# Optimization experiments

Measured on AMD Instinct MI355X. Metric: run time of the kernel, lower is better.

## Reference

```python
import jax, jax.numpy as jnp
import numpy as np

LATENT = 2048
PROJ = 128
N = 4096
TEMP = 0.5
BN_EPS = 1e-5
COS_EPS = 1e-8


def _batchnorm(x, gamma=None, beta=None):
    # training-mode BatchNorm1d: biased batch stats
    mean = jnp.mean(x, axis=0)
    var = jnp.mean((x - mean) ** 2, axis=0)
    xn = (x - mean) * jax.lax.rsqrt(var + BN_EPS)
    if gamma is not None:
        xn = xn * gamma + beta
    return xn


def _project(h, W1, gamma1, beta1, W2):
    x = h @ W1.T                      # [N, latent]
    x = jax.nn.relu(_batchnorm(x, gamma1, beta1))
    x = x @ W2.T                      # [N, proj]
    return _batchnorm(x)              # bn2 affine=False


def _normalize(z):
    n = jnp.linalg.norm(z, axis=-1, keepdims=True)
    return z / jnp.maximum(n, COS_EPS)


def setup_inputs() -> dict:
    key = jax.random.key(0)
    ks = jax.random.split(key, 4)
    scale_w1 = 1.0 / np.sqrt(LATENT)
    return {
        "h1": jax.random.normal(ks[0], (N, LATENT), jnp.float32),
        "h2": jax.random.normal(ks[1], (N, LATENT), jnp.float32),
        "W1": jax.random.normal(ks[2], (LATENT, LATENT), jnp.float32) * scale_w1,
        "gamma1": jnp.ones((LATENT,), jnp.float32),
        "beta1": jnp.zeros((LATENT,), jnp.float32),
        "W2": jax.random.normal(ks[3], (PROJ, LATENT), jnp.float32) * scale_w1,
    }


def reference(h1, h2, W1, gamma1, beta1, W2):
    z1 = _project(h1, W1, gamma1, beta1, W2)
    z2 = _project(h2, W1, gamma1, beta1, W2)
    zn1 = _normalize(z1)
    zn2 = _normalize(z2)
    inv_t = 1.0 / TEMP
    # cosine similarity as normalized GEMMs (same math as broadcast cossim)
    sim11 = (zn1 @ zn1.T) * inv_t      # [N, N]
    sim22 = (zn2 @ zn2.T) * inv_t
    sim12 = (zn1 @ zn2.T) * inv_t
    d = sim12.shape[-1]
    eye = jnp.eye(d, dtype=bool)
    neg_inf = jnp.float32(-jnp.inf)
    sim11 = jnp.where(eye, neg_inf, sim11)
    sim22 = jnp.where(eye, neg_inf, sim22)
    raw_scores1 = jnp.concatenate([sim12, sim11], axis=-1)       # [N, 2N]
    raw_scores2 = jnp.concatenate([sim22, sim12.T], axis=-1)     # [N, 2N]
    raw_scores = jnp.concatenate([raw_scores1, raw_scores2], axis=-2)  # [2N, 2N]
    targets = jnp.arange(2 * d, dtype=jnp.int64 if jax.config.jax_enable_x64 else jnp.int32)
    return raw_scores, targets
```

## Files before the change

kernel.cpp:

```cpp
#include <hip/hip_runtime.h>
#include <hip/hip_bf16.h>
#include <math.h>

#define NROWS 4096
#define MTOT  8192
#define LATENT 2048
#define PROJ 128
#define OUTN 8192
#define SPLITK 4
#define KWIN (LATENT / SPLITK)
#define CH2 256

using bf16 = __hip_bfloat16;
using bf16x8 = __attribute__((ext_vector_type(8))) short;
using bf16x4 = __attribute__((ext_vector_type(4))) short;
using f32x4  = __attribute__((ext_vector_type(4))) float;

#define LDS_AS(p) ((__attribute__((address_space(3))) void*)(p))
#define GLB_AS(p) ((const __attribute__((address_space(1))) void*)(p))

__device__ __forceinline__ float bf2f(short s) {
    return __uint_as_float(((unsigned)(unsigned short)s) << 16);
}
__device__ __forceinline__ short f2bf(float f) {
    bf16 h = __float2bfloat16(f);
    return __builtin_bit_cast(short, h);
}

__global__ void conv_all(const float* __restrict__ W1, const float* __restrict__ W2,
                         const float* __restrict__ h1, const float* __restrict__ h2,
                         bf16* __restrict__ W1b, bf16* __restrict__ W2b,
                         bf16* __restrict__ hb)
{
    const size_t g = ((size_t)blockIdx.x * 256 + threadIdx.x) * 8;
    const size_t N_W1 = (size_t)LATENT * LATENT;
    const size_t N_W2 = (size_t)PROJ * LATENT;
    const size_t N_H  = (size_t)NROWS * LATENT;
    const float* src; bf16* dst; size_t off;
    if (g < N_W1)                  { src = W1; dst = W1b;       off = g; }
    else if (g < N_W1 + N_W2)      { src = W2; dst = W2b;       off = g - N_W1; }
    else if (g < N_W1 + N_W2 + N_H){ src = h1; dst = hb;        off = g - N_W1 - N_W2; }
    else                           { src = h2; dst = hb + N_H;  off = g - N_W1 - N_W2 - N_H; }
    const float4 v0 = *reinterpret_cast<const float4*>(src + off);
    const float4 v1 = *reinterpret_cast<const float4*>(src + off + 4);
    bf16x8 o;
    o[0] = f2bf(v0.x); o[1] = f2bf(v0.y); o[2] = f2bf(v0.z); o[3] = f2bf(v0.w);
    o[4] = f2bf(v1.x); o[5] = f2bf(v1.y); o[6] = f2bf(v1.z); o[7] = f2bf(v1.w);
    *reinterpret_cast<bf16x8*>(dst + off) = o;
}

#define AREG(buf,kh) (sm + ((buf)*2 + (kh)) * 16384)
#define BREG(buf,kh) (sm + 65536 + ((buf)*2 + (kh)) * 16384)

#define LDA_(buf,kh,m) (*reinterpret_cast<const bf16x8*>(AREG(buf,kh) + (wr*128 + (m)*16 + fr)*64 + rslot))
#define LDB_(buf,kh,n) (*reinterpret_cast<const bf16x8*>(BREG(buf,kh) + (wc*64  + (n)*16 + fr)*64 + rslot))

#define STAGE_A(buf,kh,kt) do { \
    const bf16* g_ = Ag + (size_t)(bm + w*16 + srow) * 2048 + (kt)*64 + (kh)*32 + selem; \
    __builtin_amdgcn_global_load_lds(GLB_AS(g_),                  LDS_AS(AREG(buf,kh) + w*1024),        16, 0, 0); \
    __builtin_amdgcn_global_load_lds(GLB_AS(g_ + (size_t)128*2048), LDS_AS(AREG(buf,kh) + 8192 + w*1024), 16, 0, 0); \
} while(0)

#define STAGE_B(buf,kh,kt) do { \
    const bf16* g_ = Bg + (size_t)(bn + w*16 + srow) * 2048 + (kt)*64 + (kh)*32 + selem; \
    __builtin_amdgcn_global_load_lds(GLB_AS(g_),                  LDS_AS(BREG(buf,kh) + w*1024),        16, 0, 0); \
    __builtin_amdgcn_global_load_lds(GLB_AS(g_ + (size_t)128*2048), LDS_AS(BREG(buf,kh) + 8192 + w*1024), 16, 0, 0); \
} while(0)

#define PH(bufi, khi, mb, READB, STAGE_STMT, DO_VMCNT) do { \
    if (READB) { b0 = LDB_(bufi,khi,0); b1 = LDB_(bufi,khi,1); b2 = LDB_(bufi,khi,2); b3 = LDB_(bufi,khi,3); } \
    bf16x8 a0 = LDA_(bufi,khi,(mb)+0), a1 = LDA_(bufi,khi,(mb)+1), a2 = LDA_(bufi,khi,(mb)+2), a3 = LDA_(bufi,khi,(mb)+3); \
    STAGE_STMT; \
    __builtin_amdgcn_s_barrier(); \
    asm volatile("s_waitcnt lgkmcnt(0)" ::: "memory"); \
    __builtin_amdgcn_sched_barrier(0); \
    __builtin_amdgcn_s_setprio(1); \
    acc[(mb)+0][0] = __builtin_amdgcn_mfma_f32_16x16x32_bf16(b0, a0, acc[(mb)+0][0], 0,0,0); \
    acc[(mb)+0][1] = __builtin_amdgcn_mfma_f32_16x16x32_bf16(b1, a0, acc[(mb)+0][1], 0,0,0); \
    acc[(mb)+0][2] = __builtin_amdgcn_mfma_f32_16x16x32_bf16(b2, a0, acc[(mb)+0][2], 0,0,0); \
    acc[(mb)+0][3] = __builtin_amdgcn_mfma_f32_16x16x32_bf16(b3, a0, acc[(mb)+0][3], 0,0,0); \
    acc[(mb)+1][0] = __builtin_amdgcn_mfma_f32_16x16x32_bf16(b0, a1, acc[(mb)+1][0], 0,0,0); \
    acc[(mb)+1][1] = __builtin_amdgcn_mfma_f32_16x16x32_bf16(b1, a1, acc[(mb)+1][1], 0,0,0); \
    acc[(mb)+1][2] = __builtin_amdgcn_mfma_f32_16x16x32_bf16(b2, a1, acc[(mb)+1][2], 0,0,0); \
    acc[(mb)+1][3] = __builtin_amdgcn_mfma_f32_16x16x32_bf16(b3, a1, acc[(mb)+1][3], 0,0,0); \
    acc[(mb)+2][0] = __builtin_amdgcn_mfma_f32_16x16x32_bf16(b0, a2, acc[(mb)+2][0], 0,0,0); \
    acc[(mb)+2][1] = __builtin_amdgcn_mfma_f32_16x16x32_bf16(b1, a2, acc[(mb)+2][1], 0,0,0); \
    acc[(mb)+2][2] = __builtin_amdgcn_mfma_f32_16x16x32_bf16(b2, a2, acc[(mb)+2][2], 0,0,0); \
    acc[(mb)+2][3] = __builtin_amdgcn_mfma_f32_16x16x32_bf16(b3, a2, acc[(mb)+2][3], 0,0,0); \
    acc[(mb)+3][0] = __builtin_amdgcn_mfma_f32_16x16x32_bf16(b0, a3, acc[(mb)+3][0], 0,0,0); \
    acc[(mb)+3][1] = __builtin_amdgcn_mfma_f32_16x16x32_bf16(b1, a3, acc[(mb)+3][1], 0,0,0); \
    acc[(mb)+3][2] = __builtin_amdgcn_mfma_f32_16x16x32_bf16(b2, a3, acc[(mb)+3][2], 0,0,0); \
    acc[(mb)+3][3] = __builtin_amdgcn_mfma_f32_16x16x32_bf16(b3, a3, acc[(mb)+3][3], 0,0,0); \
    __builtin_amdgcn_s_setprio(0); \
    if (DO_VMCNT) { asm volatile("s_waitcnt vmcnt(6)" ::: "memory"); } \
    __builtin_amdgcn_s_barrier(); \
    __builtin_amdgcn_sched_barrier(0); \
} while (0)

__global__ __launch_bounds__(512, 2)
void gemm1_256(const bf16* __restrict__ Ag, const bf16* __restrict__ Bg,
               bf16* __restrict__ C, float* __restrict__ pS1, float* __restrict__ pSS1)
{
    extern __shared__ __align__(16) char sm[];

    const int t    = threadIdx.x;
    const int lane = t & 63;
    const int w    = t >> 6;
    const int wr   = w >> 2;
    const int wc   = w & 3;

    const int bid = blockIdx.x;
    const int lin = (bid & 7) * 32 + (bid >> 3);
    const int bm  = (lin & 31) * 256;
    const int bn  = (lin >> 5) * 256;

    const int srow  = lane >> 2;
    const int selem = 8 * ((lane & 3) ^ ((lane >> 2) & 3));
    const int fr    = lane & 15;
    const int rslot = 16 * ((lane >> 4) ^ (lane & 3));

    f32x4 acc[8][4];
#pragma unroll
    for (int m = 0; m < 8; ++m)
#pragma unroll
        for (int n = 0; n < 4; ++n)
#pragma unroll
            for (int r = 0; r < 4; ++r) acc[m][n][r] = 0.f;

    bf16x8 b0, b1, b2, b3;

    STAGE_B(0,0,0); STAGE_A(0,0,0); STAGE_B(0,1,0); STAGE_A(0,1,0);
    STAGE_B(1,0,1); STAGE_A(1,0,1); STAGE_B(1,1,1);
    asm volatile("s_waitcnt vmcnt(6)" ::: "memory");
    __builtin_amdgcn_s_barrier();
    __builtin_amdgcn_sched_barrier(0);

    for (int i = 0; i < 15; ++i) {
        const int kt1 = 2*i + 1, kt2 = 2*i + 2, kt3 = 2*i + 3;
        PH(0,0, 0, true,  STAGE_A(1,1,kt1), false);
        PH(0,0, 4, false, STAGE_B(0,0,kt2), false);
        PH(0,1, 0, true,  STAGE_A(0,0,kt2), false);
        PH(0,1, 4, false, STAGE_B(0,1,kt2), true);
        PH(1,0, 0, true,  STAGE_A(0,1,kt2), false);
        PH(1,0, 4, false, STAGE_B(1,0,kt3), false);
        PH(1,1, 0, true,  STAGE_A(1,0,kt3), false);
        PH(1,1, 4, false, STAGE_B(1,1,kt3), true);
    }

    STAGE_A(1,1,31);
    asm volatile("s_waitcnt vmcnt(0)" ::: "memory");
    __builtin_amdgcn_s_barrier();
    __builtin_amdgcn_sched_barrier(0);
    PH(0,0, 0, true,  ((void)0), false);
    PH(0,0, 4, false, ((void)0), false);
    PH(0,1, 0, true,  ((void)0), false);
    PH(0,1, 4, false, ((void)0), false);
    PH(1,0, 0, true,  ((void)0), false);
    PH(1,0, 4, false, ((void)0), false);
    PH(1,1, 0, true,  ((void)0), false);
    PH(1,1, 4, false, ((void)0), false);

    const int j_l = (lane >> 4) * 4;
#pragma unroll
    for (int m = 0; m < 8; ++m)
#pragma unroll
        for (int n = 0; n < 4; ++n) {
            const int crow = bm + wr * 128 + m * 16 + fr;
            const int ccol = bn + wc * 64 + n * 16 + j_l;
            bf16x4 o;
#pragma unroll
            for (int r = 0; r < 4; ++r) o[r] = f2bf(acc[m][n][r]);
            *reinterpret_cast<bf16x4*>(&C[(size_t)crow * LATENT + ccol]) = o;
        }

#pragma unroll
    for (int n = 0; n < 4; ++n)
#pragma unroll
        for (int r = 0; r < 4; ++r) {
            float sv = 0.f, qv = 0.f;
#pragma unroll
            for (int m = 0; m < 8; ++m) {
                const float v = acc[m][n][r];
                sv += v;
                qv = fmaf(v, v, qv);
            }
#pragma unroll
            for (int o = 1; o < 16; o <<= 1) {
                sv += __shfl_xor(sv, o);
                qv += __shfl_xor(qv, o);
            }
            if (fr == 0) {
                const int slot = ((bm >> 8) << 1) + wr;
                const int col  = bn + wc * 64 + n * 16 + j_l + r;
                pS1 [(size_t)slot * LATENT + col] = sv;
                pSS1[(size_t)slot * LATENT + col] = qv;
            }
        }
}

__global__ __launch_bounds__(512)
void gemm2_fused(const bf16* __restrict__ A, const bf16* __restrict__ B,
                 const float* __restrict__ pS1, const float* __restrict__ pSS1,
                 const float* __restrict__ gamma, const float* __restrict__ beta,
                 float* __restrict__ Part)
{
    __shared__ __align__(16) bf16 As[128 * 32];
    __shared__ __align__(16) bf16 Bs[128 * 32];
    __shared__ __align__(16) float sm_scale[KWIN];
    __shared__ __align__(16) float sm_shift[KWIN];

    const int kc = blockIdx.x;
    const int bm = blockIdx.y * 128;
    const int half = bm >> 12;
    const int kbeg = kc * KWIN;

    const int t    = threadIdx.x;
    const int lane = t & 63;
    const int w    = t >> 6;
    const int wrr  = w >> 2;
    const int wcc  = w & 3;

    {
        const int col = kbeg + t;
        float s = 0.f, ss = 0.f;
        for (int i = 0; i < 32; ++i) {
            s  += pS1 [((size_t)(half * 32 + i)) * LATENT + col];
            ss += pSS1[((size_t)(half * 32 + i)) * LATENT + col];
        }
        const float m    = s / NROWS;
        const float var  = ss / NROWS - m * m;
        const float rstd = 1.0f / sqrtf(var + 1e-5f);
        const float sc   = rstd * gamma[col];
        sm_scale[t] = sc;
        sm_shift[t] = beta[col] - m * sc;
    }
    __syncthreads();

    f32x4 acc[4][2];
#pragma unroll
    for (int m = 0; m < 4; ++m)
#pragma unroll
        for (int n = 0; n < 2; ++n)
#pragma unroll
            for (int r = 0; r < 4; ++r) acc[m][n][r] = 0.f;

    const int fr   = lane & 15;
    const int fk   = (lane >> 4) * 8;
    const int srow = t >> 2;
    const int scol = (t & 3) * 8;
    const int kend = kbeg + KWIN;

    for (int k0 = kbeg; k0 < kend; k0 += 32) {
        __builtin_amdgcn_global_load_lds(
            GLB_AS(&B[(size_t)(w * 16 + (lane >> 2)) * LATENT + k0 + (lane & 3) * 8]),
            LDS_AS(&Bs[w * 512]), 16, 0, 0);

        const int koff = k0 - kbeg;
        const float4 sc0 = *reinterpret_cast<const float4*>(&sm_scale[koff + scol]);
        const float4 sc1 = *reinterpret_cast<const float4*>(&sm_scale[koff + scol + 4]);
        const float4 sh0 = *reinterpret_cast<const float4*>(&sm_shift[koff + scol]);
        const float4 sh1 = *reinterpret_cast<const float4*>(&sm_shift[koff + scol + 4]);
        const float scv[8] = {sc0.x, sc0.y, sc0.z, sc0.w, sc1.x, sc1.y, sc1.z, sc1.w};
        const float shv[8] = {sh0.x, sh0.y, sh0.z, sh0.w, sh1.x, sh1.y, sh1.z, sh1.w};
        const bf16x8 av = *reinterpret_cast<const bf16x8*>(
            &A[(size_t)(bm + srow) * LATENT + k0 + scol]);
        bf16x8 o;
#pragma unroll
        for (int j = 0; j < 8; ++j)
            o[j] = f2bf(fmaxf(fmaf(bf2f(av[j]), scv[j], shv[j]), 0.f));
        *reinterpret_cast<bf16x8*>(&As[srow * 32 + scol]) = o;
        __syncthreads();

        bf16x8 a[4], b[2];
#pragma unroll
        for (int m = 0; m < 4; ++m)
            a[m] = *reinterpret_cast<const bf16x8*>(&As[(wrr * 64 + m * 16 + fr) * 32 + fk]);
#pragma unroll
        for (int n = 0; n < 2; ++n)
            b[n] = *reinterpret_cast<const bf16x8*>(&Bs[(wcc * 32 + n * 16 + fr) * 32 + fk]);

#pragma unroll
        for (int m = 0; m < 4; ++m)
#pragma unroll
            for (int n = 0; n < 2; ++n)
                acc[m][n] = __builtin_amdgcn_mfma_f32_16x16x32_bf16(b[n], a[m], acc[m][n], 0, 0, 0);
        __syncthreads();
    }

    const int i_l = lane & 15;
    const int j_l = (lane >> 4) * 4;
#pragma unroll
    for (int m = 0; m < 4; ++m)
#pragma unroll
        for (int n = 0; n < 2; ++n) {
            const int crow = bm + wrr * 64 + m * 16 + i_l;
            const int ccol = wcc * 32 + n * 16 + j_l;
            *reinterpret_cast<float4*>(&Part[((size_t)kc * MTOT + crow) * PROJ + ccol]) =
                make_float4(acc[m][n][0], acc[m][n][1], acc[m][n][2], acc[m][n][3]);
        }
}

__global__ __launch_bounds__(128)
void reduce2_kern(const float* __restrict__ Part, float* __restrict__ Z,
                  float* __restrict__ pS2, float* __restrict__ pSS2)
{
    const int c     = threadIdx.x;
    const int chunk = blockIdx.x;
    const int r0    = chunk * (MTOT / CH2);
    float s = 0.f, ss = 0.f;
    for (int r = r0; r < r0 + MTOT / CH2; ++r) {
        float z = 0.f;
#pragma unroll
        for (int kc = 0; kc < SPLITK; ++kc)
            z += Part[((size_t)kc * MTOT + r) * PROJ + c];
        Z[(size_t)r * PROJ + c] = z;
        s += z;
        ss = fmaf(z, z, ss);
    }
    pS2 [(size_t)chunk * PROJ + c] = s;
    pSS2[(size_t)chunk * PROJ + c] = ss;
}

__global__ __launch_bounds__(256)
void bn2_norm(const float* __restrict__ Z,
              const float* __restrict__ pS2, const float* __restrict__ pSS2,
              bf16* __restrict__ Zn, int* __restrict__ tgt)
{
    __shared__ float sm_mean[PROJ];
    __shared__ float sm_rstd[PROJ];

    const int blk  = blockIdx.x;
    const int half = blk >> 7;
    const int t    = threadIdx.x;

    if (t < PROJ) {
        float s = 0.f, ss = 0.f;
        for (int i = 0; i < CH2 / 2; ++i) {
            const int chunk = half * (CH2 / 2) + i;
            s  += pS2 [(size_t)chunk * PROJ + t];
            ss += pSS2[(size_t)chunk * PROJ + t];
        }
        const float m   = s / NROWS;
        const float var = ss / NROWS - m * m;
        sm_mean[t] = m;
        sm_rstd[t] = 1.0f / sqrtf(var + 1e-5f);
    }
    __syncthreads();

    const int lane = t & 63;
    const int sub  = t >> 6;
#pragma unroll 4
    for (int it = 0; it < 8; ++it) {
        const int row = blk * 32 + it * 4 + sub;
        const float* zr = Z + (size_t)row * PROJ;
        const float v0 = (zr[lane]      - sm_mean[lane])      * sm_rstd[lane];
        const float v1 = (zr[lane + 64] - sm_mean[lane + 64]) * sm_rstd[lane + 64];
        float ss = v0 * v0 + v1 * v1;
#pragma unroll
        for (int o = 32; o > 0; o >>= 1) ss += __shfl_xor(ss, o);
        const float inv = 1.0f / fmaxf(sqrtf(ss), 1e-8f);
        bf16* orow = Zn + (size_t)row * PROJ;
        orow[lane]      = __float2bfloat16(v0 * inv);
        orow[lane + 64] = __float2bfloat16(v1 * inv);
        if (lane == 0) tgt[row] = row;
    }
}

__global__ __launch_bounds__(256)
void sim_bf16(const bf16* __restrict__ zn, float* __restrict__ out)
{
    __shared__ __align__(16) bf16 As[4 * 128 * 32];
    __shared__ __align__(16) bf16 Bs[4 * 128 * 32];

    const int t    = threadIdx.x;
    const int lane = t & 63;
    const int w    = t >> 6;
    const int wr   = w >> 1;
    const int wc   = w & 1;
    const int bi   = blockIdx.y * 128;
    const int bj   = blockIdx.x * 128;

    const bf16* Ub = zn + (size_t)bi * PROJ;
    const bf16* Vb = zn + (size_t)(bj ^ 4096) * PROJ;

    const int srow = t >> 2;
    const int ske  = (t & 3) * 8;

#pragma unroll
    for (int q = 0; q < 4; ++q)
#pragma unroll
        for (int h = 0; h < 2; ++h) {
            const int row = h * 64 + srow;
            const int ke  = q * 32 + ske;
            __builtin_amdgcn_global_load_lds(
                GLB_AS(&Ub[(size_t)row * PROJ + ke]),
                LDS_AS(&As[q * 4096 + h * 2048 + srow * 32 + ske]), 16, 0, 0);
            __builtin_amdgcn_global_load_lds(
                GLB_AS(&Vb[(size_t)row * PROJ + ke]),
                LDS_AS(&Bs[q * 4096 + h * 2048 + srow * 32 + ske]), 16, 0, 0);
        }
    __syncthreads();

    f32x4 acc[4][4];
#pragma unroll
    for (int m = 0; m < 4; ++m)
#pragma unroll
        for (int n = 0; n < 4; ++n)
#pragma unroll
            for (int r = 0; r < 4; ++r) acc[m][n][r] = 0.f;

    const int fr = lane & 15;
    const int fk = (lane >> 4) * 8;

#pragma unroll
    for (int q = 0; q < 4; ++q) {
        bf16x8 a[4], b[4];
#pragma unroll
        for (int m = 0; m < 4; ++m)
            a[m] = *reinterpret_cast<const bf16x8*>(&As[q * 4096 + (wr * 64 + m * 16 + fr) * 32 + fk]);
#pragma unroll
        for (int n = 0; n < 4; ++n)
            b[n] = *reinterpret_cast<const bf16x8*>(&Bs[q * 4096 + (wc * 64 + n * 16 + fr) * 32 + fk]);
#pragma unroll
        for (int m = 0; m < 4; ++m)
#pragma unroll
            for (int n = 0; n < 4; ++n)
                acc[m][n] = __builtin_amdgcn_mfma_f32_16x16x32_bf16(b[n], a[m], acc[m][n], 0, 0, 0);
    }

    const int i_l = lane & 15;
    const int j_l = (lane >> 4) * 4;
#pragma unroll
    for (int m = 0; m < 4; ++m)
#pragma unroll
        for (int n = 0; n < 4; ++n) {
            const int gi  = bi + wr * 64 + m * 16 + i_l;
            const int gj0 = bj + wc * 64 + n * 16 + j_l;
            f32x4 v;
#pragma unroll
            for (int r = 0; r < 4; ++r) v[r] = acc[m][n][r] * 2.0f;
            const int mj = (gi ^ 4096) - gj0;
            if (mj >= 0 && mj < 4) v[mj] = -1.0e30f;
            __builtin_nontemporal_store(
                v, reinterpret_cast<f32x4*>(&out[(size_t)gi * OUTN + gj0]));
        }
}

extern "C" void kernel_launch(void* const* d_in, const int* in_sizes, int n_in,
                              void* d_out, int out_size, void* d_ws, size_t ws_size,
                              hipStream_t stream)
{
    const float* h1 = (const float*)d_in[0];
    const float* h2 = (const float*)d_in[1];
    const float* W1 = (const float*)d_in[2];
    const float* g1 = (const float*)d_in[3];
    const float* b1 = (const float*)d_in[4];
    const float* W2 = (const float*)d_in[5];
    float* out = (float*)d_out;

    char* p = (char*)d_ws;
    auto carve = [&](size_t bytes) { char* r = p; p += (bytes + 255) & ~(size_t)255; return r; };
    bf16*  W1b   = (bf16*) carve((size_t)LATENT * LATENT * 2);
    bf16*  W2b   = (bf16*) carve((size_t)PROJ * LATENT * 2);
    bf16*  hb    = (bf16*) carve((size_t)MTOT * LATENT * 2);
    bf16*  X     = (bf16*) carve((size_t)MTOT * LATENT * 2);
    float* Part  = (float*)carve((size_t)SPLITK * MTOT * PROJ * 4);
    float* Z     = (float*)carve((size_t)MTOT * PROJ * 4);
    bf16*  znb   = (bf16*) carve((size_t)MTOT * PROJ * 2);
    float* pS1   = (float*)carve((size_t)64 * LATENT * 4);
    float* pSS1  = (float*)carve((size_t)64 * LATENT * 4);
    float* pS2   = (float*)carve((size_t)CH2 * PROJ * 4);
    float* pSS2  = (float*)carve((size_t)CH2 * PROJ * 4);

    const int conv_groups = (LATENT * LATENT + PROJ * LATENT + 2 * NROWS * LATENT) / 8;
    conv_all<<<dim3(conv_groups / 256), 256, 0, stream>>>(W1, W2, h1, h2, W1b, W2b, hb);

    gemm1_256<<<dim3(256), 512, 131072, stream>>>(hb, W1b, X, pS1, pSS1);

    gemm2_fused<<<dim3(SPLITK, MTOT / 128), 512, 0, stream>>>(
        X, W2b, pS1, pSS1, g1, b1, Part);

    reduce2_kern<<<dim3(CH2), 128, 0, stream>>>(Part, Z, pS2, pSS2);

    int* tgt = (int*)(out + (size_t)OUTN * OUTN);
    bn2_norm<<<dim3(256), 256, 0, stream>>>(Z, pS2, pSS2, znb, tgt);

    sim_bf16<<<dim3(OUTN / 128, OUTN / 128), 256, 0, stream>>>(znb, out);
}
```

Measured before the change: 204.6 us.

## Merge gemm2, split-K reduce and BN2 normalize into one cooperative kernel

Replaces three separate launches (gemm2_fused, reduce2_kern, bn2_norm) with a single cooperative kernel of 256 blocks that uses grid.sync between phases. The goal is to remove two kernel launch gaps and tail drains in the small post-GEMM1 stages. In exchange, the grid syncs add global barrier cost, and with one 512-thread block per tile the reduce phase leaves half the threads idle.

```diff
diff --git a/kernel.cpp b/kernel.cpp
--- a/kernel.cpp
+++ b/kernel.cpp
@@ -1,6 +1,9 @@
 #include <hip/hip_runtime.h>
 #include <hip/hip_bf16.h>
+#include <hip/hip_cooperative_groups.h>
 #include <math.h>
+
+namespace cg = cooperative_groups;
 
 #define NROWS 4096
 #define MTOT  8192
@@ -199,170 +202,168 @@
 }
 
 __global__ __launch_bounds__(512)
-void gemm2_fused(const bf16* __restrict__ A, const bf16* __restrict__ B,
-                 const float* __restrict__ pS1, const float* __restrict__ pSS1,
-                 const float* __restrict__ gamma, const float* __restrict__ beta,
-                 float* __restrict__ Part)
+void tail_coop(const bf16* __restrict__ A, const bf16* __restrict__ B,
+               const float* __restrict__ pS1, const float* __restrict__ pSS1,
+               const float* __restrict__ gamma, const float* __restrict__ beta,
+               float* __restrict__ Part, float* __restrict__ Z,
+               float* __restrict__ pS2, float* __restrict__ pSS2,
+               bf16* __restrict__ Zn, int* __restrict__ tgt)
 {
     __shared__ __align__(16) bf16 As[128 * 32];
     __shared__ __align__(16) bf16 Bs[128 * 32];
     __shared__ __align__(16) float sm_scale[KWIN];
     __shared__ __align__(16) float sm_shift[KWIN];
-
-    const int kc = blockIdx.x;
-    const int bm = blockIdx.y * 128;
-    const int half = bm >> 12;
-    const int kbeg = kc * KWIN;
-
-    const int t    = threadIdx.x;
+    __shared__ float sm_mean[PROJ];
+    __shared__ float sm_rstd[PROJ];
+
+    cg::grid_group grid = cg::this_grid();
+
+    const int blk = blockIdx.x;
+    const int t   = threadIdx.x;
     const int lane = t & 63;
     const int w    = t >> 6;
-    const int wrr  = w >> 2;
-    const int wcc  = w & 3;
 
     {
-        const int col = kbeg + t;
+        const int kc   = blk & 3;
+        const int bm   = (blk >> 2) * 128;
+        const int half = bm >> 12;
+        const int kbeg = kc * KWIN;
+        const int wrr  = w >> 2;
+        const int wcc  = w & 3;
+
+        {
+            const int col = kbeg + t;
+            float s = 0.f, ss = 0.f;
+            for (int i = 0; i < 32; ++i) {
+                s  += pS1 [((size_t)(half * 32 + i)) * LATENT + col];
+                ss += pSS1[((size_t)(half * 32 + i)) * LATENT + col];
+            }
+            const float m    = s / NROWS;
+            const float var  = ss / NROWS - m * m;
+            const float rstd = 1.0f / sqrtf(var + 1e-5f);
+            const float sc   = rstd * gamma[col];
+            sm_scale[t] = sc;
+            sm_shift[t] = beta[col] - m * sc;
+        }
+        __syncthreads();
+
+        f32x4 acc[4][2];
+#pragma unroll
+        for (int m = 0; m < 4; ++m)
+#pragma unroll
+            for (int n = 0; n < 2; ++n)
+#pragma unroll
+                for (int r = 0; r < 4; ++r) acc[m][n][r] = 0.f;
+
+        const int fr   = lane & 15;
+        const int fk   = (lane >> 4) * 8;
+        const int srow = t >> 2;
+        const int scol = (t & 3) * 8;
+        const int kend = kbeg + KWIN;
+
+        for (int k0 = kbeg; k0 < kend; k0 += 32) {
+            __builtin_amdgcn_global_load_lds(
+                GLB_AS(&B[(size_t)(w * 16 + (lane >> 2)) * LATENT + k0 + (lane & 3) * 8]),
+                LDS_AS(&Bs[w * 512]), 16, 0, 0);
+
+            const int koff = k0 - kbeg;
+            const float4 sc0 = *reinterpret_cast<const float4*>(&sm_scale[koff + scol]);
+            const float4 sc1 = *reinterpret_cast<const float4*>(&sm_scale[koff + scol + 4]);
+            const float4 sh0 = *reinterpret_cast<const float4*>(&sm_shift[koff + scol]);
+            const float4 sh1 = *reinterpret_cast<const float4*>(&sm_shift[koff + scol + 4]);
+            const float scv[8] = {sc0.x, sc0.y, sc0.z, sc0.w, sc1.x, sc1.y, sc1.z, sc1.w};
+            const float shv[8] = {sh0.x, sh0.y, sh0.z, sh0.w, sh1.x, sh1.y, sh1.z, sh1.w};
+            const bf16x8 av = *reinterpret_cast<const bf16x8*>(
+                &A[(size_t)(bm + srow) * LATENT + k0 + scol]);
+            bf16x8 o;
+#pragma unroll
+            for (int j = 0; j < 8; ++j)
+                o[j] = f2bf(fmaxf(fmaf(bf2f(av[j]), scv[j], shv[j]), 0.f));
+            *reinterpret_cast<bf16x8*>(&As[srow * 32 + scol]) = o;
+            __syncthreads();
+
+            bf16x8 a[4], b[2];
+#pragma unroll
+            for (int m = 0; m < 4; ++m)
+                a[m] = *reinterpret_cast<const bf16x8*>(&As[(wrr * 64 + m * 16 + fr) * 32 + fk]);
+#pragma unroll
+            for (int n = 0; n < 2; ++n)
+                b[n] = *reinterpret_cast<const bf16x8*>(&Bs[(wcc * 32 + n * 16 + fr) * 32 + fk]);
+
+#pragma unroll
+            for (int m = 0; m < 4; ++m)
+#pragma unroll
+                for (int n = 0; n < 2; ++n)
+                    acc[m][n] = __builtin_amdgcn_mfma_f32_16x16x32_bf16(b[n], a[m], acc[m][n], 0, 0, 0);
+            __syncthreads();
+        }
+
+        const int i_l = lane & 15;
+        const int j_l = (lane >> 4) * 4;
+#pragma unroll
+        for (int m = 0; m < 4; ++m)
+#pragma unroll
+            for (int n = 0; n < 2; ++n) {
+                const int crow = bm + wrr * 64 + m * 16 + i_l;
+                const int ccol = wcc * 32 + n * 16 + j_l;
+                *reinterpret_cast<float4*>(&Part[((size_t)kc * MTOT + crow) * PROJ + ccol]) =
+                    make_float4(acc[m][n][0], acc[m][n][1], acc[m][n][2], acc[m][n][3]);
+            }
+    }
+
+    grid.sync();
+
+    if (t < 128) {
+        const int c  = t;
+        const int r0 = blk * (MTOT / CH2);
         float s = 0.f, ss = 0.f;
-        for (int i = 0; i < 32; ++i) {
-            s  += pS1 [((size_t)(half * 32 + i)) * LATENT + col];
-            ss += pSS1[((size_t)(half * 32 + i)) * LATENT + col];
-        }
-        const float m    = s / NROWS;
-        const float var  = ss / NROWS - m * m;
-        const float rstd = 1.0f / sqrtf(var + 1e-5f);
-        const float sc   = rstd * gamma[col];
-        sm_scale[t] = sc;
-        sm_shift[t] = beta[col] - m * sc;
+        for (int r = r0; r < r0 + MTOT / CH2; ++r) {
+            float z = 0.f;
+#pragma unroll
+            for (int kc = 0; kc < SPLITK; ++kc)
+                z += Part[((size_t)kc * MTOT + r) * PROJ + c];
+            Z[(size_t)r * PROJ + c] = z;
+            s += z;
+            ss = fmaf(z, z, ss);
+        }
+        pS2 [(size_t)blk * PROJ + c] = s;
+        pSS2[(size_t)blk * PROJ + c] = ss;
     }
-    __syncthreads();
-
-    f32x4 acc[4][2];
-#pragma unroll
-    for (int m = 0; m < 4; ++m)
-#pragma unroll
-        for (int n = 0; n < 2; ++n)
-#pragma unroll
-            for (int r = 0; r < 4; ++r) acc[m][n][r] = 0.f;
-
-    const int fr   = lane & 15;
-    const int fk   = (lane >> 4) * 8;
-    const int srow = t >> 2;
-    const int scol = (t & 3) * 8;
-    const int kend = kbeg + KWIN;
-
-    for (int k0 = kbeg; k0 < kend; k0 += 32) {
-        __builtin_amdgcn_global_load_lds(
-            GLB_AS(&B[(size_t)(w * 16 + (lane >> 2)) * LATENT + k0 + (lane & 3) * 8]),
-            LDS_AS(&Bs[w * 512]), 16, 0, 0);
-
-        const int koff = k0 - kbeg;
-        const float4 sc0 = *reinterpret_cast<const float4*>(&sm_scale[koff + scol]);
-        const float4 sc1 = *reinterpret_cast<const float4*>(&sm_scale[koff + scol + 4]);
-        const float4 sh0 = *reinterpret_cast<const float4*>(&sm_shift[koff + scol]);
-        const float4 sh1 = *reinterpret_cast<const float4*>(&sm_shift[koff + scol + 4]);
-        const float scv[8] = {sc0.x, sc0.y, sc0.z, sc0.w, sc1.x, sc1.y, sc1.z, sc1.w};
-        const float shv[8] = {sh0.x, sh0.y, sh0.z, sh0.w, sh1.x, sh1.y, sh1.z, sh1.w};
-        const bf16x8 av = *reinterpret_cast<const bf16x8*>(
-            &A[(size_t)(bm + srow) * LATENT + k0 + scol]);
-        bf16x8 o;
-#pragma unroll
-        for (int j = 0; j < 8; ++j)
-            o[j] = f2bf(fmaxf(fmaf(bf2f(av[j]), scv[j], shv[j]), 0.f));
-        *reinterpret_cast<bf16x8*>(&As[srow * 32 + scol]) = o;
+
+    grid.sync();
+
+    {
+        const int half = blk >> 7;
+        if (t < PROJ) {
+            float s = 0.f, ss = 0.f;
+            for (int i = 0; i < CH2 / 2; ++i) {
+                const int chunk = half * (CH2 / 2) + i;
+                s  += pS2 [(size_t)chunk * PROJ + t];
+                ss += pSS2[(size_t)chunk * PROJ + t];
+            }
+            const float m   = s / NROWS;
+            const float var = ss / NROWS - m * m;
+            sm_mean[t] = m;
+            sm_rstd[t] = 1.0f / sqrtf(var + 1e-5f);
+        }
         __syncthreads();
 
-        bf16x8 a[4], b[2];
-#pragma unroll
-        for (int m = 0; m < 4; ++m)
-            a[m] = *reinterpret_cast<const bf16x8*>(&As[(wrr * 64 + m * 16 + fr) * 32 + fk]);
-#pragma unroll
-        for (int n = 0; n < 2; ++n)
-            b[n] = *reinterpret_cast<const bf16x8*>(&Bs[(wcc * 32 + n * 16 + fr) * 32 + fk]);
-
-#pragma unroll
-        for (int m = 0; m < 4; ++m)
-#pragma unroll
-            for (int n = 0; n < 2; ++n)
-                acc[m][n] = __builtin_amdgcn_mfma_f32_16x16x32_bf16(b[n], a[m], acc[m][n], 0, 0, 0);
-        __syncthreads();
-    }
-
-    const int i_l = lane & 15;
-    const int j_l = (lane >> 4) * 4;
-#pragma unroll
-    for (int m = 0; m < 4; ++m)
-#pragma unroll
-        for (int n = 0; n < 2; ++n) {
-            const int crow = bm + wrr * 64 + m * 16 + i_l;
-            const int ccol = wcc * 32 + n * 16 + j_l;
-            *reinterpret_cast<float4*>(&Part[((size_t)kc * MTOT + crow) * PROJ + ccol]) =
-                make_float4(acc[m][n][0], acc[m][n][1], acc[m][n][2], acc[m][n][3]);
-        }
-}
-
-__global__ __launch_bounds__(128)
-void reduce2_kern(const float* __restrict__ Part, float* __restrict__ Z,
-                  float* __restrict__ pS2, float* __restrict__ pSS2)
-{
-    const int c     = threadIdx.x;
-    const int chunk = blockIdx.x;
-    const int r0    = chunk * (MTOT / CH2);
-    float s = 0.f, ss = 0.f;
-    for (int r = r0; r < r0 + MTOT / CH2; ++r) {
-        float z = 0.f;
-#pragma unroll
-        for (int kc = 0; kc < SPLITK; ++kc)
-            z += Part[((size_t)kc * MTOT + r) * PROJ + c];
-        Z[(size_t)r * PROJ + c] = z;
-        s += z;
-        ss = fmaf(z, z, ss);
-    }
-    pS2 [(size_t)chunk * PROJ + c] = s;
-    pSS2[(size_t)chunk * PROJ + c] = ss;
-}
-
-__global__ __launch_bounds__(256)
-void bn2_norm(const float* __restrict__ Z,
-              const float* __restrict__ pS2, const float* __restrict__ pSS2,
-              bf16* __restrict__ Zn, int* __restrict__ tgt)
-{
-    __shared__ float sm_mean[PROJ];
-    __shared__ float sm_rstd[PROJ];
-
-    const int blk  = blockIdx.x;
-    const int half = blk >> 7;
-    const int t    = threadIdx.x;
-
-    if (t < PROJ) {
-        float s = 0.f, ss = 0.f;
-        for (int i = 0; i < CH2 / 2; ++i) {
-            const int chunk = half * (CH2 / 2) + i;
-            s  += pS2 [(size_t)chunk * PROJ + t];
-            ss += pSS2[(size_t)chunk * PROJ + t];
-        }
-        const float m   = s / NROWS;
-        const float var = ss / NROWS - m * m;
-        sm_mean[t] = m;
-        sm_rstd[t] = 1.0f / sqrtf(var + 1e-5f);
-    }
-    __syncthreads();
-
-    const int lane = t & 63;
-    const int sub  = t >> 6;
+        const int sub = t >> 6;
 #pragma unroll 4
-    for (int it = 0; it < 8; ++it) {
-        const int row = blk * 32 + it * 4 + sub;
-        const float* zr = Z + (size_t)row * PROJ;
-        const float v0 = (zr[lane]      - sm_mean[lane])      * sm_rstd[lane];
-        const float v1 = (zr[lane + 64] - sm_mean[lane + 64]) * sm_rstd[lane + 64];
-        float ss = v0 * v0 + v1 * v1;
-#pragma unroll
-        for (int o = 32; o > 0; o >>= 1) ss += __shfl_xor(ss, o);
-        const float inv = 1.0f / fmaxf(sqrtf(ss), 1e-8f);
-        bf16* orow = Zn + (size_t)row * PROJ;
-        orow[lane]      = __float2bfloat16(v0 * inv);
-        orow[lane + 64] = __float2bfloat16(v1 * inv);
-        if (lane == 0) tgt[row] = row;
+        for (int it = 0; it < 4; ++it) {
+            const int row = blk * 32 + it * 8 + sub;
+            const float* zr = Z + (size_t)row * PROJ;
+            const float v0 = (zr[lane]      - sm_mean[lane])      * sm_rstd[lane];
+            const float v1 = (zr[lane + 64] - sm_mean[lane + 64]) * sm_rstd[lane + 64];
+            float ss = v0 * v0 + v1 * v1;
+#pragma unroll
+            for (int o = 32; o > 0; o >>= 1) ss += __shfl_xor(ss, o);
+            const float inv = 1.0f / fmaxf(sqrtf(ss), 1e-8f);
+            bf16* orow = Zn + (size_t)row * PROJ;
+            orow[lane]      = __float2bfloat16(v0 * inv);
+            orow[lane + 64] = __float2bfloat16(v1 * inv);
+            if (lane == 0) tgt[row] = row;
+        }
     }
 }
 
@@ -477,13 +478,15 @@
 
     gemm1_256<<<dim3(256), 512, 131072, stream>>>(hb, W1b, X, pS1, pSS1);
 
-    gemm2_fused<<<dim3(SPLITK, MTOT / 128), 512, 0, stream>>>(
-        X, W2b, pS1, pSS1, g1, b1, Part);
-
-    reduce2_kern<<<dim3(CH2), 128, 0, stream>>>(Part, Z, pS2, pSS2);
-
     int* tgt = (int*)(out + (size_t)OUTN * OUTN);
-    bn2_norm<<<dim3(256), 256, 0, stream>>>(Z, pS2, pSS2, znb, tgt);
+    const bf16* Xc = X; const bf16* W2c = W2b;
+    const float* pS1c = pS1; const float* pSS1c = pSS1;
+    void* args[] = {
+        (void*)&Xc, (void*)&W2c, (void*)&pS1c, (void*)&pSS1c,
+        (void*)&g1, (void*)&b1, (void*)&Part, (void*)&Z,
+        (void*)&pS2, (void*)&pSS2, (void*)&znb, (void*)&tgt
+    };
+    hipLaunchCooperativeKernel((void*)tail_coop, dim3(256), dim3(512), args, 0, stream);
 
     sim_bf16<<<dim3(OUTN / 128, OUTN / 128), 256, 0, stream>>>(znb, out);
 }
```

New measurement: 279.1 us. +36.4%, slower.
